# Performance work log

Measured on AMD Instinct MI355X. Metric: run time of the kernel, lower is better.

The kernel has to match this reference:

```python
import jax, jax.numpy as jnp
import numpy as np

LN_EPS = 1e-5


def setup_inputs() -> dict:
    key = jax.random.key(0)
    ks = jax.random.split(key, 6)
    N, E, D = 100000, 600000, 128
    x = jax.random.normal(ks[0], (N, D), dtype=jnp.float32)
    edge_index = jax.random.randint(ks[1], (2, E), 0, N, dtype=jnp.int64)
    dropout_mask = jax.random.uniform(ks[2], (N, D), dtype=jnp.float32)
    ln_gamma = jnp.ones((D,), dtype=jnp.float32)
    ln_beta = jnp.zeros((D,), dtype=jnp.float32)
    W_l = jax.random.normal(ks[3], (D, D), dtype=jnp.float32) / np.sqrt(D)
    b_l = jnp.zeros((D,), dtype=jnp.float32)
    W_r = jax.random.normal(ks[4], (D, D), dtype=jnp.float32) / np.sqrt(D)
    return {"x": x, "edge_index": edge_index, "dropout_mask": dropout_mask,
            "ln_gamma": ln_gamma, "ln_beta": ln_beta,
            "W_l": W_l, "b_l": b_l, "W_r": W_r}


def reference(x, edge_index, dropout_mask, ln_gamma, ln_beta, W_l, b_l, W_r):
    N = x.shape[0]
    # LayerNorm (elementwise affine) -> ReLU -> dropout mask
    mu = jnp.mean(x, axis=-1, keepdims=True)
    var = jnp.mean(jnp.square(x - mu), axis=-1, keepdims=True)
    h = (x - mu) * jax.lax.rsqrt(var + LN_EPS) * ln_gamma + ln_beta
    h = jax.nn.relu(h) * dropout_mask  # [N, D]
    # SAGEConv with mean aggregation: messages flow src -> dst
    src, dst = edge_index[0], edge_index[1]
    agg = jax.ops.segment_sum(h[src], dst, num_segments=N)  # [N, D]
    cnt = jax.ops.segment_sum(jnp.ones_like(dst, dtype=h.dtype), dst,
                              num_segments=N)
    mean_agg = agg / jnp.maximum(cnt, 1.0)[:, None]
    # out = lin_l(mean_agg) + lin_r(h); PyG stores weights as [out, in]
    return mean_agg @ W_l.T + b_l + h @ W_r.T
```

## Files before the change

### kernel.cpp

```cpp
#include <hip/hip_runtime.h>

#define LN_EPS 1e-5f
#define D 128
#define SCAN_CHUNK 1024
#define LDSA_STRIDE 264

typedef __attribute__((ext_vector_type(4))) float f32x4;
typedef __attribute__((ext_vector_type(8))) short bf16x8;

static __device__ __forceinline__ ushort f2bf(float f) {
    union { float f; unsigned u; } a; a.f = f;
    unsigned r = a.u + 0x7FFF + ((a.u >> 16) & 1);
    return (ushort)(r >> 16);
}
static __device__ __forceinline__ float bf2f(ushort u) {
    union { unsigned u; float f; } a; a.u = ((unsigned)u) << 16;
    return a.f;
}

__global__ void prep_w(const float* __restrict__ Wl,
                       const float* __restrict__ Wr,
                       ushort* __restrict__ Bfrag,
                       int* __restrict__ hist,
                       int* __restrict__ csums, int N) {
    int t = blockIdx.x * blockDim.x + threadIdx.x;
    if (t < 8 * 8 * 64 * 8) {
        int i    = t & 7;
        int lane = (t >> 3) & 63;
        int jb   = (t >> 9) & 7;
        int ks   = t >> 12;
        int k = ks * 32 + (lane >> 4) * 8 + i;
        int j = jb * 16 + (lane & 15);
        float v = (k < D) ? Wl[j * D + k] : Wr[j * D + (k - D)];
        Bfrag[t] = f2bf(v);
    }
    if (t < 128) csums[t] = 0;
    for (int i = t; i < N; i += gridDim.x * blockDim.x) hist[i] = 0;
}

__global__ void ln_hist(const float* __restrict__ x,
                        const float* __restrict__ mask,
                        const float* __restrict__ gamma,
                        const float* __restrict__ beta,
                        ushort* __restrict__ hbf,
                        const int* __restrict__ ei,
                        int* __restrict__ hist,
                        int N, int E, int lnBlocks) {
    if ((int)blockIdx.x >= lnBlocks) {
        int base = (((int)blockIdx.x - lnBlocks) * 256 + (int)threadIdx.x) * 4;
        const int* dst = ei + E;
        if (base + 3 < E) {
            int4 d = *(const int4*)(dst + base);
            atomicAdd(&hist[d.x], 1);
            atomicAdd(&hist[d.y], 1);
            atomicAdd(&hist[d.z], 1);
            atomicAdd(&hist[d.w], 1);
        } else {
            for (int i = base; i < E && i < base + 4; i++)
                atomicAdd(&hist[dst[i]], 1);
        }
        return;
    }
    int tid  = threadIdx.x;
    int lane = tid & 63;
    int wid  = ((int)blockIdx.x * 256 + tid) >> 6;
    int g2   = lane >> 4;
    int sl   = lane & 15;
    int node = wid * 4 + g2;
    if (node >= N) return;

    const float* xr = x + (size_t)node * D + sl * 8;
    f32x4 v0 = *(const f32x4*)xr;
    f32x4 v1 = *(const f32x4*)(xr + 4);
    const float* mr = mask + (size_t)node * D + sl * 8;
    f32x4 m0 = *(const f32x4*)mr;
    f32x4 m1 = *(const f32x4*)(mr + 4);

    float s  = (v0.x + v0.y) + (v0.z + v0.w) + (v1.x + v1.y) + (v1.z + v1.w);
    float ss = (v0.x * v0.x + v0.y * v0.y) + (v0.z * v0.z + v0.w * v0.w)
             + (v1.x * v1.x + v1.y * v1.y) + (v1.z * v1.z + v1.w * v1.w);
#pragma unroll
    for (int off = 8; off > 0; off >>= 1) {
        s  += __shfl_xor(s, off);
        ss += __shfl_xor(ss, off);
    }
    float mu  = s * (1.0f / D);
    float var = ss * (1.0f / D) - mu * mu;
    float rs  = rsqrtf(var + LN_EPS);

    f32x4 g0 = *(const f32x4*)(gamma + sl * 8);
    f32x4 g1 = *(const f32x4*)(gamma + sl * 8 + 4);
    f32x4 b0 = *(const f32x4*)(beta + sl * 8);
    f32x4 b1 = *(const f32x4*)(beta + sl * 8 + 4);

    bf16x8 o;
    o[0] = (short)f2bf(fmaxf((v0.x - mu) * rs * g0.x + b0.x, 0.0f) * m0.x);
    o[1] = (short)f2bf(fmaxf((v0.y - mu) * rs * g0.y + b0.y, 0.0f) * m0.y);
    o[2] = (short)f2bf(fmaxf((v0.z - mu) * rs * g0.z + b0.z, 0.0f) * m0.z);
    o[3] = (short)f2bf(fmaxf((v0.w - mu) * rs * g0.w + b0.w, 0.0f) * m0.w);
    o[4] = (short)f2bf(fmaxf((v1.x - mu) * rs * g1.x + b1.x, 0.0f) * m1.x);
    o[5] = (short)f2bf(fmaxf((v1.y - mu) * rs * g1.y + b1.y, 0.0f) * m1.y);
    o[6] = (short)f2bf(fmaxf((v1.z - mu) * rs * g1.z + b1.z, 0.0f) * m1.z);
    o[7] = (short)f2bf(fmaxf((v1.w - mu) * rs * g1.w + b1.w, 0.0f) * m1.w);
    *(bf16x8*)(hbf + (size_t)node * D + sl * 8) = o;
}

__global__ void scan_all(const int* __restrict__ hist, int* __restrict__ offs,
                         int* __restrict__ cursor, int* __restrict__ csums, int N) {
    __shared__ int lds[256];
    __shared__ int base_s;
    int base = blockIdx.x * SCAN_CHUNK;
    int t = threadIdx.x;
    int idx0 = base + t * 4;
    int v[4];
#pragma unroll
    for (int i = 0; i < 4; i++) {
        int idx = idx0 + i;
        v[i] = (idx < N) ? hist[idx] : 0;
    }
    lds[t] = v[0] + v[1] + v[2] + v[3];
    __syncthreads();
    for (int off = 1; off < 256; off <<= 1) {
        int add = (t >= off) ? lds[t - off] : 0;
        __syncthreads();
        lds[t] += add;
        __syncthreads();
    }
    int run = (t == 0) ? 0 : lds[t - 1];
    if (t == 255)
        __hip_atomic_store(&csums[blockIdx.x], lds[255] | 0x40000000,
                           __ATOMIC_RELEASE, __HIP_MEMORY_SCOPE_AGENT);
    if (t < 64) {
        int acc = 0;
        for (int c = t; c < (int)blockIdx.x; c += 64) {
            int w;
            do {
                w = __hip_atomic_load(&csums[c], __ATOMIC_ACQUIRE,
                                      __HIP_MEMORY_SCOPE_AGENT);
            } while (!(w & 0x40000000));
            acc += w & 0x3FFFFFFF;
        }
#pragma unroll
        for (int off = 32; off > 0; off >>= 1) acc += __shfl_xor(acc, off);
        if (t == 0) base_s = acc;
    }
    __syncthreads();
    run += base_s;
#pragma unroll
    for (int i = 0; i < 4; i++) {
        int idx = idx0 + i;
        if (idx < N) {
            offs[idx] = run;
            cursor[idx] = run;
        }
        run += v[i];
    }
}

__global__ void sort_edges(const int* __restrict__ ei, int* __restrict__ cursor,
                           int* __restrict__ sorted_src, int E) {
    int e = blockIdx.x * blockDim.x + threadIdx.x;
    if (e >= E) return;
    int dst = ei[E + e];
    int pos = atomicAdd(&cursor[dst], 1);
    sorted_src[pos] = ei[e];
}

__global__ void __launch_bounds__(256, 4)
agg_gemm(float* __restrict__ out,
         const ushort* __restrict__ hbf,
         const int* __restrict__ sorted_src,
         const int* __restrict__ offs,
         const int* __restrict__ hist,
         const ushort* __restrict__ Bfrag,
         const float* __restrict__ bl,
         int N, int E) {
    __shared__ ushort Alds[64 * LDSA_STRIDE];
    int tid  = threadIdx.x;
    int wave = tid >> 6;
    int lane = tid & 63;
    int n0 = blockIdx.x * 64;

#pragma unroll
    for (int it = 0; it < 4; it++) {
        int chunk = tid + 256 * it;
        int row = chunk >> 4;
        int c8  = chunk & 15;
        int node = n0 + row;
        bf16x8 vh = (bf16x8){0,0,0,0,0,0,0,0};
        if (node < N) vh = *(const bf16x8*)(hbf + (size_t)node * D + c8 * 8);
        *(bf16x8*)&Alds[row * LDSA_STRIDE + 128 + c8 * 8] = vh;
    }

    int g  = lane >> 4;
    int sl = lane & 15;
    int row0 = wave * 16 + g;
    int start[4], deg[4], dm1[4];
#pragma unroll
    for (int p = 0; p < 4; p++) {
        int node = n0 + row0 + p * 4;
        start[p] = 0; deg[p] = 0;
        if (node < N) { start[p] = offs[node]; deg[p] = hist[node]; }
        dm1[p] = deg[p] - 1; if (dm1[p] < 0) dm1[p] = 0;
    }
    float acc[4][8];
#pragma unroll
    for (int p = 0; p < 4; p++)
#pragma unroll
        for (int q = 0; q < 8; q++) acc[p][q] = 0.0f;

    int dmax = max(max(deg[0], deg[1]), max(deg[2], deg[3]));
    int Em = E - 1;
    int idx[4][4];
#pragma unroll
    for (int k = 0; k < 4; k++)
#pragma unroll
        for (int p = 0; p < 4; p++) {
            int jc = (k < dm1[p]) ? k : dm1[p];
            int pos = start[p] + jc; if (pos > Em) pos = Em;
            idx[k][p] = sorted_src[pos];
        }
    for (int j = 0; j < dmax; j += 4) {
        int cur[4][4];
#pragma unroll
        for (int k = 0; k < 4; k++)
#pragma unroll
            for (int p = 0; p < 4; p++) cur[k][p] = idx[k][p];
#pragma unroll
        for (int k = 0; k < 4; k++)
#pragma unroll
            for (int p = 0; p < 4; p++) {
                int jn = j + 4 + k; jn = (jn < dm1[p]) ? jn : dm1[p];
                int pos = start[p] + jn; if (pos > Em) pos = Em;
                idx[k][p] = sorted_src[pos];
            }
#pragma unroll
        for (int k = 0; k < 4; k++) {
#pragma unroll
            for (int p = 0; p < 4; p++) {
                bf16x8 v = *(const bf16x8*)(hbf + (size_t)cur[k][p] * D + sl * 8);
                float m = (j + k < deg[p]) ? 1.0f : 0.0f;
#pragma unroll
                for (int q = 0; q < 8; q++) acc[p][q] += bf2f((ushort)v[q]) * m;
            }
        }
    }
#pragma unroll
    for (int p = 0; p < 4; p++) {
        float inv = 1.0f / fmaxf((float)deg[p], 1.0f);
        bf16x8 o;
#pragma unroll
        for (int q = 0; q < 8; q++) o[q] = (short)f2bf(acc[p][q] * inv);
        *(bf16x8*)&Alds[(row0 + p * 4) * LDSA_STRIDE + sl * 8] = o;
    }
    __syncthreads();

    bf16x8 breg[8][2];
#pragma unroll
    for (int ks = 0; ks < 8; ks++)
#pragma unroll
        for (int jj = 0; jj < 2; jj++) {
            int jb = wave * 2 + jj;
            breg[ks][jj] = *(const bf16x8*)(Bfrag + (size_t)((ks * 8 + jb) * 64 + lane) * 8);
        }

    f32x4 acc2[4][2];
#pragma unroll
    for (int nb = 0; nb < 4; nb++)
#pragma unroll
        for (int jj = 0; jj < 2; jj++)
            acc2[nb][jj] = (f32x4){0.f, 0.f, 0.f, 0.f};

    int arow = lane & 15;
    int akoff = (lane >> 4) * 8;
#pragma unroll
    for (int ks = 0; ks < 8; ks++) {
#pragma unroll
        for (int nb = 0; nb < 4; nb++) {
            bf16x8 a = *(const bf16x8*)&Alds[(nb * 16 + arow) * LDSA_STRIDE + ks * 32 + akoff];
            acc2[nb][0] = __builtin_amdgcn_mfma_f32_16x16x32_bf16(a, breg[ks][0], acc2[nb][0], 0, 0, 0);
            acc2[nb][1] = __builtin_amdgcn_mfma_f32_16x16x32_bf16(a, breg[ks][1], acc2[nb][1], 0, 0, 0);
        }
    }

    float bias0 = bl[wave * 32 + (lane & 15)];
    float bias1 = bl[wave * 32 + 16 + (lane & 15)];
    int rbase = (lane >> 4) * 4;
#pragma unroll
    for (int nb = 0; nb < 4; nb++) {
#pragma unroll
        for (int r = 0; r < 4; r++) {
            int row = nb * 16 + rbase + r;
            if (n0 + row < N) {
                float* orow = out + (size_t)(n0 + row) * D + wave * 32 + (lane & 15);
                orow[0]  = acc2[nb][0][r] + bias0;
                orow[16] = acc2[nb][1][r] + bias1;
            }
        }
    }
}

extern "C" void kernel_launch(void* const* d_in, const int* in_sizes, int n_in,
                              void* d_out, int out_size, void* d_ws, size_t ws_size,
                              hipStream_t stream) {
    const float* x     = (const float*)d_in[0];
    const int*   ei    = (const int*)  d_in[1];
    const float* mask  = (const float*)d_in[2];
    const float* gamma = (const float*)d_in[3];
    const float* beta  = (const float*)d_in[4];
    const float* Wl    = (const float*)d_in[5];
    const float* bl    = (const float*)d_in[6];
    const float* Wr    = (const float*)d_in[7];
    float* out = (float*)d_out;

    int N = in_sizes[0] / D;
    int E = in_sizes[1] / 2;
    int chunks = (N + SCAN_CHUNK - 1) / SCAN_CHUNK;

    ushort* hbf   = (ushort*)d_ws;
    ushort* Bfrag = hbf + (size_t)N * D;
    int* hist   = (int*)(Bfrag + 32768);
    int* offs   = hist + N;
    int* cursor = offs + N;
    int* csums  = cursor + N;
    int* ssrc   = csums + 128;

    int lnBlocks   = (N + 15) / 16;
    int histBlocks = (E + 1023) / 1024;

    prep_w<<<512, 256, 0, stream>>>(Wl, Wr, Bfrag, hist, csums, N);
    ln_hist<<<lnBlocks + histBlocks, 256, 0, stream>>>(x, mask, gamma, beta, hbf,
                                                       ei, hist, N, E, lnBlocks);
    scan_all<<<chunks, 256, 0, stream>>>(hist, offs, cursor, csums, N);
    sort_edges<<<(E + 255) / 256, 256, 0, stream>>>(ei, cursor, ssrc, E);
    agg_gemm<<<(N + 63) / 64, 256, 0, stream>>>(out, hbf, ssrc, offs, hist, Bfrag,
                                                bl, N, E);
}
```

Measured before the change: 297.0 us.

## Split LayerNorm from histogram, vectorize edge sort, shorten gather prefetch depth

Splits the fused LayerNorm and histogram kernel into two kernels. LayerNorm now runs after the edge sort, just before aggregation, so the bf16 features are freshly written when they are gathered. The edge sort now handles four edges per thread with int4 loads. The aggregation loop prefetches two neighbor indices per row instead of four, which should lower register pressure but also leaves fewer gathers in flight. The extra kernel launch and the loss of overlap between LayerNorm and the histogram are the costs.

```diff
diff --git a/kernel.cpp b/kernel.cpp
--- a/kernel.cpp
+++ b/kernel.cpp
@@ -38,71 +38,19 @@
     for (int i = t; i < N; i += gridDim.x * blockDim.x) hist[i] = 0;
 }
 
-__global__ void ln_hist(const float* __restrict__ x,
-                        const float* __restrict__ mask,
-                        const float* __restrict__ gamma,
-                        const float* __restrict__ beta,
-                        ushort* __restrict__ hbf,
-                        const int* __restrict__ ei,
-                        int* __restrict__ hist,
-                        int N, int E, int lnBlocks) {
-    if ((int)blockIdx.x >= lnBlocks) {
-        int base = (((int)blockIdx.x - lnBlocks) * 256 + (int)threadIdx.x) * 4;
-        const int* dst = ei + E;
-        if (base + 3 < E) {
-            int4 d = *(const int4*)(dst + base);
-            atomicAdd(&hist[d.x], 1);
-            atomicAdd(&hist[d.y], 1);
-            atomicAdd(&hist[d.z], 1);
-            atomicAdd(&hist[d.w], 1);
-        } else {
-            for (int i = base; i < E && i < base + 4; i++)
-                atomicAdd(&hist[dst[i]], 1);
-        }
-        return;
-    }
-    int tid  = threadIdx.x;
-    int lane = tid & 63;
-    int wid  = ((int)blockIdx.x * 256 + tid) >> 6;
-    int g2   = lane >> 4;
-    int sl   = lane & 15;
-    int node = wid * 4 + g2;
-    if (node >= N) return;
-
-    const float* xr = x + (size_t)node * D + sl * 8;
-    f32x4 v0 = *(const f32x4*)xr;
-    f32x4 v1 = *(const f32x4*)(xr + 4);
-    const float* mr = mask + (size_t)node * D + sl * 8;
-    f32x4 m0 = *(const f32x4*)mr;
-    f32x4 m1 = *(const f32x4*)(mr + 4);
-
-    float s  = (v0.x + v0.y) + (v0.z + v0.w) + (v1.x + v1.y) + (v1.z + v1.w);
-    float ss = (v0.x * v0.x + v0.y * v0.y) + (v0.z * v0.z + v0.w * v0.w)
-             + (v1.x * v1.x + v1.y * v1.y) + (v1.z * v1.z + v1.w * v1.w);
-#pragma unroll
-    for (int off = 8; off > 0; off >>= 1) {
-        s  += __shfl_xor(s, off);
-        ss += __shfl_xor(ss, off);
-    }
-    float mu  = s * (1.0f / D);
-    float var = ss * (1.0f / D) - mu * mu;
-    float rs  = rsqrtf(var + LN_EPS);
-
-    f32x4 g0 = *(const f32x4*)(gamma + sl * 8);
-    f32x4 g1 = *(const f32x4*)(gamma + sl * 8 + 4);
-    f32x4 b0 = *(const f32x4*)(beta + sl * 8);
-    f32x4 b1 = *(const f32x4*)(beta + sl * 8 + 4);
-
-    bf16x8 o;
-    o[0] = (short)f2bf(fmaxf((v0.x - mu) * rs * g0.x + b0.x, 0.0f) * m0.x);
-    o[1] = (short)f2bf(fmaxf((v0.y - mu) * rs * g0.y + b0.y, 0.0f) * m0.y);
-    o[2] = (short)f2bf(fmaxf((v0.z - mu) * rs * g0.z + b0.z, 0.0f) * m0.z);
-    o[3] = (short)f2bf(fmaxf((v0.w - mu) * rs * g0.w + b0.w, 0.0f) * m0.w);
-    o[4] = (short)f2bf(fmaxf((v1.x - mu) * rs * g1.x + b1.x, 0.0f) * m1.x);
-    o[5] = (short)f2bf(fmaxf((v1.y - mu) * rs * g1.y + b1.y, 0.0f) * m1.y);
-    o[6] = (short)f2bf(fmaxf((v1.z - mu) * rs * g1.z + b1.z, 0.0f) * m1.z);
-    o[7] = (short)f2bf(fmaxf((v1.w - mu) * rs * g1.w + b1.w, 0.0f) * m1.w);
-    *(bf16x8*)(hbf + (size_t)node * D + sl * 8) = o;
+__global__ void hist_k(const int* __restrict__ ei, int* __restrict__ hist, int E) {
+    int base = (blockIdx.x * blockDim.x + threadIdx.x) * 4;
+    const int* dst = ei + E;
+    if (base + 3 < E) {
+        int4 d = *(const int4*)(dst + base);
+        atomicAdd(&hist[d.x], 1);
+        atomicAdd(&hist[d.y], 1);
+        atomicAdd(&hist[d.z], 1);
+        atomicAdd(&hist[d.w], 1);
+    } else {
+        for (int i = base; i < E && i < base + 4; i++)
+            atomicAdd(&hist[dst[i]], 1);
+    }
 }
 
 __global__ void scan_all(const int* __restrict__ hist, int* __restrict__ offs,
@@ -159,11 +107,74 @@
 
 __global__ void sort_edges(const int* __restrict__ ei, int* __restrict__ cursor,
                            int* __restrict__ sorted_src, int E) {
-    int e = blockIdx.x * blockDim.x + threadIdx.x;
-    if (e >= E) return;
-    int dst = ei[E + e];
-    int pos = atomicAdd(&cursor[dst], 1);
-    sorted_src[pos] = ei[e];
+    int base = (blockIdx.x * blockDim.x + threadIdx.x) * 4;
+    if (base >= E) return;
+    if (base + 3 < E) {
+        int4 d = *(const int4*)(ei + E + base);
+        int4 s = *(const int4*)(ei + base);
+        int p0 = atomicAdd(&cursor[d.x], 1);
+        int p1 = atomicAdd(&cursor[d.y], 1);
+        int p2 = atomicAdd(&cursor[d.z], 1);
+        int p3 = atomicAdd(&cursor[d.w], 1);
+        sorted_src[p0] = s.x;
+        sorted_src[p1] = s.y;
+        sorted_src[p2] = s.z;
+        sorted_src[p3] = s.w;
+    } else {
+        for (int e = base; e < E; e++) {
+            int pos = atomicAdd(&cursor[ei[E + e]], 1);
+            sorted_src[pos] = ei[e];
+        }
+    }
+}
+
+__global__ void ln_k(const float* __restrict__ x,
+                     const float* __restrict__ mask,
+                     const float* __restrict__ gamma,
+                     const float* __restrict__ beta,
+                     ushort* __restrict__ hbf, int N) {
+    int tid  = threadIdx.x;
+    int lane = tid & 63;
+    int wid  = ((int)blockIdx.x * 256 + tid) >> 6;
+    int g2   = lane >> 4;
+    int sl   = lane & 15;
+    int node = wid * 4 + g2;
+    if (node >= N) return;
+
+    const float* xr = x + (size_t)node * D + sl * 8;
+    f32x4 v0 = *(const f32x4*)xr;
+    f32x4 v1 = *(const f32x4*)(xr + 4);
+    const float* mr = mask + (size_t)node * D + sl * 8;
+    f32x4 m0 = *(const f32x4*)mr;
+    f32x4 m1 = *(const f32x4*)(mr + 4);
+
+    float s  = (v0.x + v0.y) + (v0.z + v0.w) + (v1.x + v1.y) + (v1.z + v1.w);
+    float ss = (v0.x * v0.x + v0.y * v0.y) + (v0.z * v0.z + v0.w * v0.w)
+             + (v1.x * v1.x + v1.y * v1.y) + (v1.z * v1.z + v1.w * v1.w);
+#pragma unroll
+    for (int off = 8; off > 0; off >>= 1) {
+        s  += __shfl_xor(s, off);
+        ss += __shfl_xor(ss, off);
+    }
+    float mu  = s * (1.0f / D);
+    float var = ss * (1.0f / D) - mu * mu;
+    float rs  = rsqrtf(var + LN_EPS);
+
+    f32x4 g0 = *(const f32x4*)(gamma + sl * 8);
+    f32x4 g1 = *(const f32x4*)(gamma + sl * 8 + 4);
+    f32x4 b0 = *(const f32x4*)(beta + sl * 8);
+    f32x4 b1 = *(const f32x4*)(beta + sl * 8 + 4);
+
+    bf16x8 o;
+    o[0] = (short)f2bf(fmaxf((v0.x - mu) * rs * g0.x + b0.x, 0.0f) * m0.x);
+    o[1] = (short)f2bf(fmaxf((v0.y - mu) * rs * g0.y + b0.y, 0.0f) * m0.y);
+    o[2] = (short)f2bf(fmaxf((v0.z - mu) * rs * g0.z + b0.z, 0.0f) * m0.z);
+    o[3] = (short)f2bf(fmaxf((v0.w - mu) * rs * g0.w + b0.w, 0.0f) * m0.w);
+    o[4] = (short)f2bf(fmaxf((v1.x - mu) * rs * g1.x + b1.x, 0.0f) * m1.x);
+    o[5] = (short)f2bf(fmaxf((v1.y - mu) * rs * g1.y + b1.y, 0.0f) * m1.y);
+    o[6] = (short)f2bf(fmaxf((v1.z - mu) * rs * g1.z + b1.z, 0.0f) * m1.z);
+    o[7] = (short)f2bf(fmaxf((v1.w - mu) * rs * g1.w + b1.w, 0.0f) * m1.w);
+    *(bf16x8*)(hbf + (size_t)node * D + sl * 8) = o;
 }
 
 __global__ void __launch_bounds__(256, 4)
@@ -211,38 +222,41 @@
 
     int dmax = max(max(deg[0], deg[1]), max(deg[2], deg[3]));
     int Em = E - 1;
-    int idx[4][4];
-#pragma unroll
-    for (int k = 0; k < 4; k++)
+    int ia[4], ib[4];
+#pragma unroll
+    for (int p = 0; p < 4; p++) {
+        int pa = start[p];                         if (pa > Em) pa = Em;
+        int j1 = (1 < dm1[p]) ? 1 : dm1[p];
+        int pb = start[p] + j1;                    if (pb > Em) pb = Em;
+        ia[p] = sorted_src[pa];
+        ib[p] = sorted_src[pb];
+    }
+    for (int j = 0; j < dmax; j += 2) {
+        int ca[4], cb[4];
+#pragma unroll
+        for (int p = 0; p < 4; p++) { ca[p] = ia[p]; cb[p] = ib[p]; }
 #pragma unroll
         for (int p = 0; p < 4; p++) {
-            int jc = (k < dm1[p]) ? k : dm1[p];
-            int pos = start[p] + jc; if (pos > Em) pos = Em;
-            idx[k][p] = sorted_src[pos];
-        }
-    for (int j = 0; j < dmax; j += 4) {
-        int cur[4][4];
-#pragma unroll
-        for (int k = 0; k < 4; k++)
-#pragma unroll
-            for (int p = 0; p < 4; p++) cur[k][p] = idx[k][p];
-#pragma unroll
-        for (int k = 0; k < 4; k++)
-#pragma unroll
-            for (int p = 0; p < 4; p++) {
-                int jn = j + 4 + k; jn = (jn < dm1[p]) ? jn : dm1[p];
-                int pos = start[p] + jn; if (pos > Em) pos = Em;
-                idx[k][p] = sorted_src[pos];
-            }
-#pragma unroll
-        for (int k = 0; k < 4; k++) {
-#pragma unroll
-            for (int p = 0; p < 4; p++) {
-                bf16x8 v = *(const bf16x8*)(hbf + (size_t)cur[k][p] * D + sl * 8);
-                float m = (j + k < deg[p]) ? 1.0f : 0.0f;
-#pragma unroll
-                for (int q = 0; q < 8; q++) acc[p][q] += bf2f((ushort)v[q]) * m;
-            }
+            int j2 = (j + 2 < dm1[p]) ? j + 2 : dm1[p];
+            int j3 = (j + 3 < dm1[p]) ? j + 3 : dm1[p];
+            int pa = start[p] + j2; if (pa > Em) pa = Em;
+            int pb = start[p] + j3; if (pb > Em) pb = Em;
+            ia[p] = sorted_src[pa];
+            ib[p] = sorted_src[pb];
+        }
+#pragma unroll
+        for (int p = 0; p < 4; p++) {
+            bf16x8 v = *(const bf16x8*)(hbf + (size_t)ca[p] * D + sl * 8);
+            float m = (j < deg[p]) ? 1.0f : 0.0f;
+#pragma unroll
+            for (int q = 0; q < 8; q++) acc[p][q] += bf2f((ushort)v[q]) * m;
+        }
+#pragma unroll
+        for (int p = 0; p < 4; p++) {
+            bf16x8 v = *(const bf16x8*)(hbf + (size_t)cb[p] * D + sl * 8);
+            float m = (j + 1 < deg[p]) ? 1.0f : 0.0f;
+#pragma unroll
+            for (int q = 0; q < 8; q++) acc[p][q] += bf2f((ushort)v[q]) * m;
         }
     }
 #pragma unroll
@@ -325,14 +339,11 @@
     int* csums  = cursor + N;
     int* ssrc   = csums + 128;
 
-    int lnBlocks   = (N + 15) / 16;
-    int histBlocks = (E + 1023) / 1024;
-
     prep_w<<<512, 256, 0, stream>>>(Wl, Wr, Bfrag, hist, csums, N);
-    ln_hist<<<lnBlocks + histBlocks, 256, 0, stream>>>(x, mask, gamma, beta, hbf,
-                                                       ei, hist, N, E, lnBlocks);
+    hist_k<<<(E / 4 + 255) / 256, 256, 0, stream>>>(ei, hist, E);
     scan_all<<<chunks, 256, 0, stream>>>(hist, offs, cursor, csums, N);
-    sort_edges<<<(E + 255) / 256, 256, 0, stream>>>(ei, cursor, ssrc, E);
+    sort_edges<<<(E / 4 + 255) / 256, 256, 0, stream>>>(ei, cursor, ssrc, E);
+    ln_k<<<(N + 15) / 16, 256, 0, stream>>>(x, mask, gamma, beta, hbf, N);
     agg_gemm<<<(N + 63) / 64, 256, 0, stream>>>(out, hbf, ssrc, offs, hist, Bfrag,
                                                 bl, N, E);
 }
```

Result: faster. 261.3 us (-12.0%).
